# Kernel optimization log

Hardware: AMD Instinct MI355X
Metric: run time of the kernel (lower is better)

The kernel has to match this reference:

```python
import jax, jax.numpy as jnp
import numpy as np

N = 4194304          # total elements
NUM_IDS = 262144     # sorted ids drawn from [0, NUM_IDS)
M_CAP = NUM_IDS + 1  # static upper bound on number of runs (sorted input)
L_CAP = 128          # static upper bound on run length (safe for this distribution)


def setup_inputs() -> dict:
    key = jax.random.key(0)
    k1, k2 = jax.random.split(key)
    ids = jnp.sort(jax.random.randint(k1, (N,), 0, NUM_IDS, dtype=jnp.int32))
    features = jax.random.normal(k2, (N,), dtype=jnp.float32)
    return {"ids": ids, "features": features}


def _group(ids, features):
    """Run-length grouping of consecutive equal ids into a padded [M_CAP, L_CAP] layout.
    Faithful to the tf.scan original: the FINAL run is never emitted (it stays in state).
    Rows beyond the valid runs are zero-filled; their ids are -1 (the original's sentinel).
    """
    n = ids.shape[0]
    ar = jnp.arange(n, dtype=jnp.int32)
    # boundary detection -> run index per element via prefix sum
    is_start = jnp.concatenate([jnp.ones((1,), bool), ids[1:] != ids[:-1]])
    seg = jnp.cumsum(is_start.astype(jnp.int32)) - 1      # [N] run id per element
    num_runs = seg[-1] + 1
    valid_seg = seg < (num_runs - 1)                        # drop last run (scan never emits it)
    # start position of each run (segment-min of element index)
    starts = jnp.full((M_CAP,), n, dtype=jnp.int32).at[seg].min(ar)
    pos = ar - starts[seg]                                  # [N] position within run
    ok = valid_seg & (pos < L_CAP)
    seg_idx = jnp.where(ok, seg, M_CAP)                     # out-of-range -> dropped
    padded = jnp.zeros((M_CAP, L_CAP), features.dtype).at[seg_idx, pos].set(features, mode='drop')
    run_ids = jnp.full((M_CAP,), -1, dtype=ids.dtype).at[jnp.where(valid_seg, seg, M_CAP)].set(ids, mode='drop')
    return run_ids, padded


def reference(ids, features):
    return _group(ids, features)
```

## Files before the change

### kernel.cpp

```cpp
#include <hip/hip_runtime.h>
#include <hip/hip_bf16.h>

#define N_ELEM   4194304
#define NUM_IDS  262144
#define M_CAP    (NUM_IDS + 1)
#define L_CAP    128

#define SCAN_BLOCKS 256

__global__ void k_boundaries(const int* __restrict__ ids,
                             int* __restrict__ start_arr,
                             int* __restrict__ end_arr,
                             int* __restrict__ present,
                             int n) {
    int i = blockIdx.x * blockDim.x + threadIdx.x;
    if (i >= n) return;
    int v = ids[i];
    if (i == 0 || ids[i - 1] != v) {
        start_arr[v] = i;
        present[v]   = 1;
    }
    if (i == n - 1 || ids[i + 1] != v)
        end_arr[v] = i + 1;
}

__global__ void k_scan_blocks(const int* __restrict__ present,
                              int* __restrict__ rank_local,
                              int* __restrict__ partial) {
    int b = blockIdx.x, t = threadIdx.x;
    int4 p = ((const int4*)present)[b * 256 + t];
    int s1 = p.x + p.y;
    int s2 = s1 + p.z;
    int tsum = s2 + p.w;

    __shared__ int sm[256];
    sm[t] = tsum;
    __syncthreads();
    for (int off = 1; off < 256; off <<= 1) {
        int val = (t >= off) ? sm[t - off] : 0;
        __syncthreads();
        if (t >= off) sm[t] += val;
        __syncthreads();
    }
    int excl = sm[t] - tsum;

    int4 r;
    r.x = excl;
    r.y = excl + p.x;
    r.z = excl + s1;
    r.w = excl + s2;
    ((int4*)rank_local)[b * 256 + t] = r;

    if (t == 255) partial[b] = sm[255];
}

__global__ void k_scan_partials(const int* __restrict__ partial,
                                int* __restrict__ offsets,
                                int* __restrict__ num_runs) {
    int t = threadIdx.x;
    int v = partial[t];
    __shared__ int sm[256];
    sm[t] = v;
    __syncthreads();
    for (int off = 1; off < 256; off <<= 1) {
        int val = (t >= off) ? sm[t - off] : 0;
        __syncthreads();
        if (t >= off) sm[t] += val;
        __syncthreads();
    }
    offsets[t] = sm[t] - v;
    if (t == 255) num_runs[0] = sm[255];
}

__global__ void k_scatter(const int* __restrict__ present,
                          const int* __restrict__ rank_local,
                          const int* __restrict__ offsets,
                          int* __restrict__ row_id) {
    int v = blockIdx.x * blockDim.x + threadIdx.x;
    if (v >= NUM_IDS) return;
    if (present[v])
        row_id[rank_local[v] + offsets[v >> 10]] = v;
}

__global__ void k_write_rows(const int* __restrict__ row_id,
                             const int* __restrict__ start_arr,
                             const int* __restrict__ end_arr,
                             const int* __restrict__ num_runs_ptr,
                             const float* __restrict__ feat,
                             float* __restrict__ out) {
    int wave = threadIdx.x >> 6;
    int lane = threadIdx.x & 63;
    int m = blockIdx.x * 4 + wave;
    if (m >= M_CAP) return;

    int num_valid = num_runs_ptr[0] - 1;
    float* row = out + M_CAP + (size_t)m * L_CAP;

    if (m < num_valid) {
        int v = row_id[m];
        int s = start_arr[v];
        int len = end_arr[v] - s;
        if (len > L_CAP) len = L_CAP;
        if (lane == 0) out[m] = (float)v;
        float e0 = (lane < len)      ? feat[s + lane]      : 0.0f;
        float e1 = (lane + 64 < len) ? feat[s + lane + 64] : 0.0f;
        row[lane]      = e0;
        row[lane + 64] = e1;
    } else {
        if (lane == 0) out[m] = -1.0f;
        row[lane]      = 0.0f;
        row[lane + 64] = 0.0f;
    }
}

extern "C" void kernel_launch(void* const* d_in, const int* in_sizes, int n_in,
                              void* d_out, int out_size, void* d_ws, size_t ws_size,
                              hipStream_t stream) {
    const int n = in_sizes[0];
    const int* ids = (const int*)d_in[0];
    const float* feat = (const float*)d_in[1];
    float* out = (float*)d_out;

    int* ws        = (int*)d_ws;
    int* start_arr = ws;
    int* end_arr   = start_arr + NUM_IDS;
    int* present   = end_arr   + NUM_IDS;
    int* rank_loc  = present   + NUM_IDS;
    int* partial   = rank_loc  + NUM_IDS;
    int* offsets   = partial   + 256;
    int* num_runs  = offsets   + 256;
    int* row_id    = num_runs  + 4;

    hipMemsetAsync(present, 0, NUM_IDS * sizeof(int), stream);

    k_boundaries<<<(n + 255) / 256, 256, 0, stream>>>(ids, start_arr, end_arr, present, n);
    k_scan_blocks<<<SCAN_BLOCKS, 256, 0, stream>>>(present, rank_loc, partial);
    k_scan_partials<<<1, 256, 0, stream>>>(partial, offsets, num_runs);
    k_scatter<<<NUM_IDS / 256, 256, 0, stream>>>(present, rank_loc, offsets, row_id);
    k_write_rows<<<(M_CAP + 3) / 4, 256, 0, stream>>>(row_id, start_arr, end_arr,
                                                      num_runs, feat, out);
}
```

Before: 225.7 us.

## Fuse all stages into one cooperative kernel with element-order run scan

Replaces the five-kernel pipeline and memset with a single cooperative kernel that uses grid syncs between phases. Run starts are found by scanning boundary flags per element (16 per thread) rather than through per-id present/start/end tables, so run starts and ids are compacted directly in order. The output is then written as aligned float4 stores over the whole padded buffer. This removes launch overhead, the memset and the id-indexed intermediate traffic, at the cost of three grid-wide barriers and a cooperative-launch residency requirement for 1024 blocks.

```diff
diff --git a/kernel.cpp b/kernel.cpp
--- a/kernel.cpp
+++ b/kernel.cpp
@@ -1,142 +1,171 @@
 #include <hip/hip_runtime.h>
-#include <hip/hip_bf16.h>
+#include <hip/hip_cooperative_groups.h>
+
+namespace cg = cooperative_groups;
 
 #define N_ELEM   4194304
 #define NUM_IDS  262144
 #define M_CAP    (NUM_IDS + 1)
 #define L_CAP    128
 
-#define SCAN_BLOCKS 256
+#define NBLK 1024
+#define NTHR 256
+#define TOTAL_THREADS (NBLK * NTHR)
+#define EPT 16
 
-__global__ void k_boundaries(const int* __restrict__ ids,
-                             int* __restrict__ start_arr,
-                             int* __restrict__ end_arr,
-                             int* __restrict__ present,
-                             int n) {
-    int i = blockIdx.x * blockDim.x + threadIdx.x;
-    if (i >= n) return;
-    int v = ids[i];
-    if (i == 0 || ids[i - 1] != v) {
-        start_arr[v] = i;
-        present[v]   = 1;
+#define P_TOTAL   (M_CAP * L_CAP)
+#define OUT_TOTAL (M_CAP + P_TOTAL)
+#define Q0        (M_CAP + 3)
+#define NF4       ((OUT_TOTAL - Q0) / 4)
+
+__global__ void __launch_bounds__(NTHR, 1)
+k_fused(const int* __restrict__ ids,
+        const float* __restrict__ feat,
+        float* __restrict__ out,
+        int* __restrict__ ws) {
+    int* partial    = ws;
+    int* offsets    = ws + NBLK;
+    int* num_runs_p = ws + 2 * NBLK;
+    int* run_start  = ws + 2 * NBLK + 4;
+    int* run_vid    = run_start + 262148;
+
+    const int b = blockIdx.x, t = threadIdx.x;
+    const int gtid = b * NTHR + t;
+    cg::grid_group grid = cg::this_grid();
+    __shared__ int sm[NTHR];
+
+    const int base = gtid * EPT;
+    int v[EPT];
+    {
+        const int4* p4 = (const int4*)(ids + base);
+        int4 a = p4[0], b4 = p4[1], c4 = p4[2], d4 = p4[3];
+        v[0]=a.x; v[1]=a.y; v[2]=a.z; v[3]=a.w;
+        v[4]=b4.x; v[5]=b4.y; v[6]=b4.z; v[7]=b4.w;
+        v[8]=c4.x; v[9]=c4.y; v[10]=c4.z; v[11]=c4.w;
+        v[12]=d4.x; v[13]=d4.y; v[14]=d4.z; v[15]=d4.w;
     }
-    if (i == n - 1 || ids[i + 1] != v)
-        end_arr[v] = i + 1;
-}
+    const int prev = (gtid == 0) ? -1 : ids[base - 1];
 
-__global__ void k_scan_blocks(const int* __restrict__ present,
-                              int* __restrict__ rank_local,
-                              int* __restrict__ partial) {
-    int b = blockIdx.x, t = threadIdx.x;
-    int4 p = ((const int4*)present)[b * 256 + t];
-    int s1 = p.x + p.y;
-    int s2 = s1 + p.z;
-    int tsum = s2 + p.w;
+    int c = 0;
+    int flag[EPT];
+#pragma unroll
+    for (int j = 0; j < EPT; ++j) {
+        flag[j] = (v[j] != ((j == 0) ? prev : v[j - 1]));
+        c += flag[j];
+    }
 
-    __shared__ int sm[256];
-    sm[t] = tsum;
+    sm[t] = c;
     __syncthreads();
-    for (int off = 1; off < 256; off <<= 1) {
+    for (int off = 1; off < NTHR; off <<= 1) {
         int val = (t >= off) ? sm[t - off] : 0;
         __syncthreads();
         if (t >= off) sm[t] += val;
         __syncthreads();
     }
-    int excl = sm[t] - tsum;
+    const int texcl = sm[t] - c;
+    if (t == NTHR - 1) partial[b] = sm[NTHR - 1];
 
-    int4 r;
-    r.x = excl;
-    r.y = excl + p.x;
-    r.z = excl + s1;
-    r.w = excl + s2;
-    ((int4*)rank_local)[b * 256 + t] = r;
+    grid.sync();
 
-    if (t == 255) partial[b] = sm[255];
-}
+    if (b == 0) {
+        int4 pp = ((const int4*)partial)[t];
+        int s1 = pp.x + pp.y, s2 = s1 + pp.z, tsum = s2 + pp.w;
+        sm[t] = tsum;
+        __syncthreads();
+        for (int off = 1; off < NTHR; off <<= 1) {
+            int val = (t >= off) ? sm[t - off] : 0;
+            __syncthreads();
+            if (t >= off) sm[t] += val;
+            __syncthreads();
+        }
+        int excl = sm[t] - tsum;
+        int4 r;
+        r.x = excl; r.y = excl + pp.x; r.z = excl + s1; r.w = excl + s2;
+        ((int4*)offsets)[t] = r;
+        if (t == NTHR - 1) num_runs_p[0] = sm[NTHR - 1];
+    }
 
-__global__ void k_scan_partials(const int* __restrict__ partial,
-                                int* __restrict__ offsets,
-                                int* __restrict__ num_runs) {
-    int t = threadIdx.x;
-    int v = partial[t];
-    __shared__ int sm[256];
-    sm[t] = v;
-    __syncthreads();
-    for (int off = 1; off < 256; off <<= 1) {
-        int val = (t >= off) ? sm[t - off] : 0;
-        __syncthreads();
-        if (t >= off) sm[t] += val;
-        __syncthreads();
+    grid.sync();
+
+    {
+        int rank = offsets[b] + texcl;
+#pragma unroll
+        for (int j = 0; j < EPT; ++j) {
+            if (flag[j]) {
+                run_start[rank] = base + j;
+                run_vid[rank]   = v[j];
+                ++rank;
+            }
+        }
     }
-    offsets[t] = sm[t] - v;
-    if (t == 255) num_runs[0] = sm[255];
-}
 
-__global__ void k_scatter(const int* __restrict__ present,
-                          const int* __restrict__ rank_local,
-                          const int* __restrict__ offsets,
-                          int* __restrict__ row_id) {
-    int v = blockIdx.x * blockDim.x + threadIdx.x;
-    if (v >= NUM_IDS) return;
-    if (present[v])
-        row_id[rank_local[v] + offsets[v >> 10]] = v;
-}
+    grid.sync();
 
-__global__ void k_write_rows(const int* __restrict__ row_id,
-                             const int* __restrict__ start_arr,
-                             const int* __restrict__ end_arr,
-                             const int* __restrict__ num_runs_ptr,
-                             const float* __restrict__ feat,
-                             float* __restrict__ out) {
-    int wave = threadIdx.x >> 6;
-    int lane = threadIdx.x & 63;
-    int m = blockIdx.x * 4 + wave;
-    if (m >= M_CAP) return;
+    const int num_valid = num_runs_p[0] - 1;
 
-    int num_valid = num_runs_ptr[0] - 1;
-    float* row = out + M_CAP + (size_t)m * L_CAP;
+    {
+        int rv = run_vid[gtid];
+        out[gtid] = (gtid < num_valid) ? (float)rv : -1.0f;
+    }
 
-    if (m < num_valid) {
-        int v = row_id[m];
-        int s = start_arr[v];
-        int len = end_arr[v] - s;
-        if (len > L_CAP) len = L_CAP;
-        if (lane == 0) out[m] = (float)v;
-        float e0 = (lane < len)      ? feat[s + lane]      : 0.0f;
-        float e1 = (lane + 64 < len) ? feat[s + lane + 64] : 0.0f;
-        row[lane]      = e0;
-        row[lane + 64] = e1;
-    } else {
-        if (lane == 0) out[m] = -1.0f;
-        row[lane]      = 0.0f;
-        row[lane + 64] = 0.0f;
+    if (gtid == 0) {
+        out[M_CAP - 1] = -1.0f;
+        int s0 = 0, len0 = 0;
+        if (num_valid > 0) {
+            s0 = run_start[0];
+            int e0 = run_start[1];
+            len0 = min(e0 - s0, L_CAP);
+        }
+#pragma unroll
+        for (int p = 0; p < 3; ++p)
+            out[M_CAP + p] = (p < len0) ? feat[s0 + p] : 0.0f;
+        out[OUT_TOTAL - 1] = 0.0f;
+    }
+
+    for (int k = gtid; k < NF4; k += TOTAL_THREADS) {
+        const int p  = 3 + 4 * k;
+        const int m0 = p >> 7;
+        const int m3 = (p + 3) >> 7;
+
+        int s0 = 0, len0 = 0;
+        if (m0 < num_valid) {
+            s0 = run_start[m0];
+            len0 = min(run_start[m0 + 1] - s0, L_CAP);
+        }
+        int s3 = s0, len3 = len0;
+        if (m3 != m0) {
+            s3 = 0; len3 = 0;
+            if (m3 < num_valid) {
+                s3 = run_start[m3];
+                len3 = min(run_start[m3 + 1] - s3, L_CAP);
+            }
+        }
+
+        float4 r;
+        {
+            int pj, cj, s, L;
+            pj = p;     cj = pj & 127; s = (pj>>7)==m0 ? s0 : s3; L = (pj>>7)==m0 ? len0 : len3;
+            r.x = (cj < L) ? feat[s + cj] : 0.0f;
+            pj = p + 1; cj = pj & 127; s = (pj>>7)==m0 ? s0 : s3; L = (pj>>7)==m0 ? len0 : len3;
+            r.y = (cj < L) ? feat[s + cj] : 0.0f;
+            pj = p + 2; cj = pj & 127; s = (pj>>7)==m0 ? s0 : s3; L = (pj>>7)==m0 ? len0 : len3;
+            r.z = (cj < L) ? feat[s + cj] : 0.0f;
+            pj = p + 3; cj = pj & 127; s = (pj>>7)==m0 ? s0 : s3; L = (pj>>7)==m0 ? len0 : len3;
+            r.w = (cj < L) ? feat[s + cj] : 0.0f;
+        }
+        *(float4*)(out + Q0 + 4 * (size_t)k) = r;
     }
 }
 
 extern "C" void kernel_launch(void* const* d_in, const int* in_sizes, int n_in,
                               void* d_out, int out_size, void* d_ws, size_t ws_size,
                               hipStream_t stream) {
-    const int n = in_sizes[0];
     const int* ids = (const int*)d_in[0];
     const float* feat = (const float*)d_in[1];
     float* out = (float*)d_out;
+    int* ws = (int*)d_ws;
 
-    int* ws        = (int*)d_ws;
-    int* start_arr = ws;
-    int* end_arr   = start_arr + NUM_IDS;
-    int* present   = end_arr   + NUM_IDS;
-    int* rank_loc  = present   + NUM_IDS;
-    int* partial   = rank_loc  + NUM_IDS;
-    int* offsets   = partial   + 256;
-    int* num_runs  = offsets   + 256;
-    int* row_id    = num_runs  + 4;
-
-    hipMemsetAsync(present, 0, NUM_IDS * sizeof(int), stream);
-
-    k_boundaries<<<(n + 255) / 256, 256, 0, stream>>>(ids, start_arr, end_arr, present, n);
-    k_scan_blocks<<<SCAN_BLOCKS, 256, 0, stream>>>(present, rank_loc, partial);
-    k_scan_partials<<<1, 256, 0, stream>>>(partial, offsets, num_runs);
-    k_scatter<<<NUM_IDS / 256, 256, 0, stream>>>(present, rank_loc, offsets, row_id);
-    k_write_rows<<<(M_CAP + 3) / 4, 256, 0, stream>>>(row_id, start_arr, end_arr,
-                                                      num_runs, feat, out);
+    void* args[] = { (void*)&ids, (void*)&feat, (void*)&out, (void*)&ws };
+    hipLaunchCooperativeKernel((void*)k_fused, dim3(NBLK), dim3(NTHR),
+                               args, 0, stream);
 }
```

After: 489.6 us. +116.9%, slower.
